# Performance work log

Measured on AMD Instinct MI355X. Metric: run time of the kernel, lower is better.

The kernel has to match this reference:

```python
import jax, jax.numpy as jnp
import numpy as np

K = 4          # deform conv kernel size
STRIDE = 4     # deform conv stride (no padding)
EPS = 1e-5     # BatchNorm eps
SLOPE = 0.01   # LeakyReLU default negative slope


def conv2d(x, w, b, stride):
    out = jax.lax.conv_general_dilated(
        x, w, (stride, stride), 'VALID',
        dimension_numbers=('NCHW', 'OIHW', 'NCHW'))
    return out + b[None, :, None, None]


def batchnorm(x, g, b, m, v):
    inv = g / jnp.sqrt(v + EPS)
    return x * inv[None, :, None, None] + (b - m * inv)[None, :, None, None]


def leaky_relu(x):
    return jnp.where(x >= 0, x, SLOPE * x)


def deform_conv(x, offset, w, b):
    # x: [B,C,H,W], offset: [B,2*K*K,Ho,Wo] with (dy,dx) interleaved per kernel tap
    B, C, H, W = x.shape
    Ho, Wo = offset.shape[2], offset.shape[3]
    KK = K * K
    off = offset.reshape(B, KK, 2, Ho, Wo)
    kh = jnp.repeat(jnp.arange(K), K).astype(x.dtype)   # [KK] kernel row
    kw = jnp.tile(jnp.arange(K), K).astype(x.dtype)     # [KK] kernel col
    base_y = (jnp.arange(Ho) * STRIDE).astype(x.dtype)
    base_x = (jnp.arange(Wo) * STRIDE).astype(x.dtype)
    # sampling coordinates [B,KK,Ho,Wo]
    py = base_y[None, None, :, None] + kh[None, :, None, None] + off[:, :, 0]
    px = base_x[None, None, None, :] + kw[None, :, None, None] + off[:, :, 1]
    y0 = jnp.floor(py)
    x0 = jnp.floor(px)
    wy = py - y0
    wx = px - x0

    def corner(yc, xc):
        yi = yc.astype(jnp.int32)
        xi = xc.astype(jnp.int32)
        valid = (yi >= 0) & (yi < H) & (xi >= 0) & (xi < W)
        yi = jnp.clip(yi, 0, H - 1)
        xi = jnp.clip(xi, 0, W - 1)
        # per-batch gather: [B,C,KK,Ho,Wo]
        v = jax.vmap(lambda img, a, c: img[:, a, c])(x, yi, xi)
        return v * valid[:, None].astype(x.dtype)

    v00 = corner(y0, x0)
    v01 = corner(y0, x0 + 1)
    v10 = corner(y0 + 1, x0)
    v11 = corner(y0 + 1, x0 + 1)
    wy_ = wy[:, None]
    wx_ = wx[:, None]
    sampled = (v00 * (1 - wy_) * (1 - wx_) + v01 * (1 - wy_) * wx_
               + v10 * wy_ * (1 - wx_) + v11 * wy_ * wx_)  # [B,C,KK,Ho,Wo]
    out = jnp.einsum('bckhw,ock->bohw', sampled, w.reshape(w.shape[0], C, KK))
    return out + b[None, :, None, None]


def setup_inputs() -> dict:
    key = jax.random.key(0)
    ks = jax.random.split(key, 16)
    f32 = jnp.float32
    inp = {
        'x': jax.random.normal(ks[0], (64, 3, 224, 224), f32),
        'stem_w': jax.random.normal(ks[1], (96, 3, 4, 4), f32) * 0.1,
        'stem_b': jax.random.normal(ks[2], (96,), f32) * 0.05,
        'bn1_g': jax.random.uniform(ks[3], (96,), f32, 0.5, 1.5),
        'bn1_b': jax.random.normal(ks[4], (96,), f32) * 0.05,
        'bn1_m': jax.random.normal(ks[5], (96,), f32) * 0.05,
        'bn1_v': jax.random.uniform(ks[6], (96,), f32, 0.5, 1.5),
        'off_w': jax.random.normal(ks[7], (32, 96, 4, 4), f32) * 0.02,
        'off_b': jax.random.normal(ks[8], (32,), f32) * 0.02,
        'dcn_w': jax.random.normal(ks[9], (768, 96, 4, 4), f32) * 0.05,
        'dcn_b': jax.random.normal(ks[10], (768,), f32) * 0.05,
        'bn2_g': jax.random.uniform(ks[11], (768,), f32, 0.5, 1.5),
        'bn2_b': jax.random.normal(ks[12], (768,), f32) * 0.05,
        'bn2_m': jax.random.normal(ks[13], (768,), f32) * 0.05,
        'bn2_v': jax.random.uniform(ks[14], (768,), f32, 0.5, 1.5),
    }
    return inp


def reference(x, stem_w, stem_b, bn1_g, bn1_b, bn1_m, bn1_v,
              off_w, off_b, dcn_w, dcn_b, bn2_g, bn2_b, bn2_m, bn2_v):
    h = conv2d(x, stem_w, stem_b, 4)                      # [B,96,56,56]
    h = leaky_relu(batchnorm(h, bn1_g, bn1_b, bn1_m, bn1_v))
    offset = conv2d(h, off_w, off_b, 4)                   # [B,32,14,14]
    h = deform_conv(h, offset, dcn_w, dcn_b)              # [B,768,14,14]
    h = leaky_relu(batchnorm(h, bn2_g, bn2_b, bn2_m, bn2_v))
    B, C, Ho, Wo = h.shape
    return h.reshape(B, C, Ho * Wo).transpose(0, 2, 1)    # [B,196,768]
```

## Files before the change

kernel.cpp:

```cpp
#include <hip/hip_runtime.h>

#define EPS   1e-5f
#define SLOPE 0.01f

#define WS_H1B  0L
#define WS_OFF  9633792L
#define WS_W1T  10035200L
#define WS_S1   10039808L
#define WS_T1   10039904L
#define WS_T2   10040000L
#define WS_SB   10040768L
#define WS_WTB  19674560L
#define WS_WOB  20264384L

__device__ __forceinline__ unsigned short f2bf(float f) {
    unsigned int u = __builtin_bit_cast(unsigned int, f);
    u += 0x7fffu + ((u >> 16) & 1u);
    return (unsigned short)(u >> 16);
}
__device__ __forceinline__ float bf2f(unsigned short u) {
    unsigned int t = ((unsigned int)u) << 16;
    return __builtin_bit_cast(float, t);
}

typedef __attribute__((ext_vector_type(4))) unsigned short ushort4v;
typedef __attribute__((ext_vector_type(8))) short bf16x8;
typedef __attribute__((ext_vector_type(4))) float floatx4;

__global__ __launch_bounds__(256) void k0_prep(
    const float* __restrict__ stem_w, const float* __restrict__ stem_b,
    const float* __restrict__ bn1_g,  const float* __restrict__ bn1_b,
    const float* __restrict__ bn1_m,  const float* __restrict__ bn1_v,
    const float* __restrict__ off_w,  const float* __restrict__ dcn_w,
    const float* __restrict__ dcn_b,  const float* __restrict__ bn2_g,
    const float* __restrict__ bn2_b,  const float* __restrict__ bn2_m,
    const float* __restrict__ bn2_v,  float* __restrict__ ws)
{
    long i = (long)blockIdx.x * 256 + threadIdx.x;
    unsigned short* Wtb = (unsigned short*)(ws + WS_WTB);
    unsigned short* Wob = (unsigned short*)(ws + WS_WOB);
    if (i < 1179648L) {
        int oc = (int)(i / 1536), k = (int)(i % 1536);
        int kk = k / 96, c = k % 96;
        float inv2 = bn2_g[oc] * rsqrtf(bn2_v[oc] + EPS);
        Wtb[i] = f2bf(dcn_w[oc * 1536 + c * 16 + kk] * inv2);
    } else if (i < 1228800L) {
        int i2 = (int)(i - 1179648L);
        int oc = i2 / 1536, k = i2 % 1536;
        int khw = k / 96, c = k % 96;
        Wob[i2] = f2bf(off_w[oc * 1536 + c * 16 + khw]);
    } else if (i < 1233408L) {
        int i3 = (int)(i - 1228800L);
        int k = i3 / 96, c = i3 % 96;
        ws[WS_W1T + i3] = stem_w[c * 48 + k];
    } else if (i < 1233504L) {
        int c = (int)(i - 1233408L);
        ws[WS_S1 + c] = bn1_g[c] * rsqrtf(bn1_v[c] + EPS);
    } else if (i < 1233600L) {
        int c = (int)(i - 1233504L);
        float s = bn1_g[c] * rsqrtf(bn1_v[c] + EPS);
        ws[WS_T1 + c] = stem_b[c] * s + bn1_b[c] - bn1_m[c] * s;
    } else if (i < 1234368L) {
        int oc = (int)(i - 1233600L);
        float inv2 = bn2_g[oc] * rsqrtf(bn2_v[oc] + EPS);
        ws[WS_T2 + oc] = dcn_b[oc] * inv2 + bn2_b[oc] - bn2_m[oc] * inv2;
    }
}

__global__ __launch_bounds__(384) void k1_stem(
    const float* __restrict__ x, const float* __restrict__ w1t,
    const float* __restrict__ s1, const float* __restrict__ t1,
    unsigned short* __restrict__ h1)
{
    const int oy = blockIdx.x;
    const int b  = blockIdx.y;
    const int tid = threadIdx.x;

    __shared__ float xs[3 * 4 * 224];
    __shared__ float wsh[48 * 100];
    __shared__ float s1s[96], t1s[96];

    for (int i = tid; i < 2688; i += 384) {
        int ci = i / 896, r = i % 896;
        int kh = r / 224, xx = r % 224;
        xs[i] = x[((long)(b * 3 + ci) * 224 + oy * 4 + kh) * 224 + xx];
    }
    for (int i = tid; i < 4608; i += 384) {
        int k = i / 96, c = i % 96;
        wsh[k * 100 + c] = w1t[i];
    }
    if (tid < 96) { s1s[tid] = s1[tid]; t1s[tid] = t1[tid]; }
    __syncthreads();

    if (tid < 336) {
        int oxg = tid / 24, cg = tid % 24;
        float acc[4][4] = {};
#pragma unroll
        for (int ci = 0; ci < 3; ci++) {
#pragma unroll
            for (int kh = 0; kh < 4; kh++) {
                const float* xrow = &xs[(ci * 4 + kh) * 224 + oxg * 16];
                float4 xv[4], wv[4];
#pragma unroll
                for (int o = 0; o < 4; o++) xv[o] = *(const float4*)&xrow[o * 4];
#pragma unroll
                for (int kw = 0; kw < 4; kw++)
                    wv[kw] = *(const float4*)&wsh[(ci * 16 + kh * 4 + kw) * 100 + cg * 4];
#pragma unroll
                for (int kw = 0; kw < 4; kw++) {
                    const float* wf = (const float*)&wv[kw];
#pragma unroll
                    for (int o = 0; o < 4; o++) {
                        float xv_s = ((const float*)&xv[o])[kw];
#pragma unroll
                        for (int cc = 0; cc < 4; cc++)
                            acc[o][cc] += xv_s * wf[cc];
                    }
                }
            }
        }
#pragma unroll
        for (int o = 0; o < 4; o++) {
            ushort4v hp;
#pragma unroll
            for (int cc = 0; cc < 4; cc++) {
                int c = cg * 4 + cc;
                float v = acc[o][cc] * s1s[c] + t1s[c];
                v = v >= 0.f ? v : SLOPE * v;
                ((unsigned short*)&hp)[cc] = f2bf(v);
            }
            *(ushort4v*)&h1[((long)((b * 56 + oy) * 56) + oxg * 4 + o) * 96 + cg * 4] = hp;
        }
    }
}

__global__ __launch_bounds__(256) void k2_mfma(
    const unsigned short* __restrict__ h1,
    const unsigned short* __restrict__ Wob,
    const float* __restrict__ off_b, float* __restrict__ off)
{
    const int tid  = threadIdx.x;
    const int wave = tid >> 6;
    const int lane = tid & 63;
    const int n0   = blockIdx.x * 128;
    const int m    = lane & 15;
    const int quad = lane >> 4;

    __shared__ unsigned short sA[128 * 32];
    __shared__ unsigned short sB[32 * 32];

    const int skoff = (lane & 3) * 8;
    int n_a = n0 + wave * 32 + (lane >> 2);
    int n_b = n_a + 16;
    int ba = n_a / 196, pa = n_a % 196;
    int bb = n_b / 196, pb = n_b % 196;
    long pixa = ((long)(ba * 56 + (pa / 14) * 4) * 56 + (pa % 14) * 4);
    long pixb = ((long)(bb * 56 + (pb / 14) * 4) * 56 + (pb % 14) * 4);

    const unsigned short* gB = Wob + (long)((wave & 1) * 16 + (lane >> 2)) * 1536 + skoff;
    unsigned short* lA0 = &sA[(wave * 32 +  0) * 32];
    unsigned short* lA1 = &sA[(wave * 32 + 16) * 32];
    unsigned short* lB  = &sB[((wave & 1) * 16) * 32];

    floatx4 acc[2][2];
#pragma unroll
    for (int i = 0; i < 2; i++)
#pragma unroll
        for (int j = 0; j < 2; j++) acc[i][j] = (floatx4)0.f;

    for (int kt = 0; kt < 48; ++kt) {
        int khw = kt / 3;
        int c0  = (kt - khw * 3) * 32;
        int kh  = khw >> 2, kw = khw & 3;
        long eoff = (long)(kh * 56 + kw) * 96 + c0 + skoff;
        const unsigned short* gA0 = h1 + pixa * 96 + eoff;
        const unsigned short* gA1 = h1 + pixb * 96 + eoff;

        __syncthreads();
        __builtin_amdgcn_global_load_lds(
            (const __attribute__((address_space(1))) void*)gA0,
            (__attribute__((address_space(3))) void*)lA0, 16, 0, 0);
        __builtin_amdgcn_global_load_lds(
            (const __attribute__((address_space(1))) void*)gA1,
            (__attribute__((address_space(3))) void*)lA1, 16, 0, 0);
        if (wave < 2)
            __builtin_amdgcn_global_load_lds(
                (const __attribute__((address_space(1))) void*)gB,
                (__attribute__((address_space(3))) void*)lB, 16, 0, 0);
        gB += 32;
        __syncthreads();

        bf16x8 af[2], bfr[2];
#pragma unroll
        for (int i = 0; i < 2; i++)
            af[i] = *(const bf16x8*)&sA[(wave * 32 + i * 16 + m) * 32 + quad * 8];
#pragma unroll
        for (int j = 0; j < 2; j++)
            bfr[j] = *(const bf16x8*)&sB[(j * 16 + m) * 32 + quad * 8];
#pragma unroll
        for (int i = 0; i < 2; i++)
#pragma unroll
            for (int j = 0; j < 2; j++)
                acc[i][j] = __builtin_amdgcn_mfma_f32_16x16x32_bf16(
                    af[i], bfr[j], acc[i][j], 0, 0, 0);
    }

    float tb[2];
#pragma unroll
    for (int j = 0; j < 2; j++) tb[j] = off_b[j * 16 + m];
#pragma unroll
    for (int i = 0; i < 2; i++)
#pragma unroll
        for (int r = 0; r < 4; r++) {
            long n = n0 + wave * 32 + i * 16 + quad * 4 + r;
#pragma unroll
            for (int j = 0; j < 2; j++)
                off[n * 32 + j * 16 + m] = acc[i][j][r] + tb[j];
        }
}

__global__ __launch_bounds__(384) void k3_sample(
    const unsigned short* __restrict__ h1, const float* __restrict__ off,
    unsigned short* __restrict__ S)
{
    const int p = blockIdx.x;
    const int b = blockIdx.y;
    const int y = p / 14, xo = p % 14;
    const int tid = threadIdx.x;
    const int c4 = tid % 24, kk = tid / 24;
    const int kh = kk >> 2, kw = kk & 3;

    const float* ob = off + ((long)(b * 196 + p)) * 32;
    float dy = ob[kk * 2];
    float dx = ob[kk * 2 + 1];

    float py = (float)(y * 4 + kh) + dy;
    float px = (float)(xo * 4 + kw) + dx;
    float y0f = floorf(py), x0f = floorf(px);
    float wy = py - y0f, wx = px - x0f;
    int y0 = (int)y0f, x0 = (int)x0f;
    int y1 = y0 + 1,  x1 = x0 + 1;

    float my0 = (y0 >= 0 && y0 < 56) ? 1.f : 0.f;
    float my1 = (y1 >= 0 && y1 < 56) ? 1.f : 0.f;
    float mx0 = (x0 >= 0 && x0 < 56) ? 1.f : 0.f;
    float mx1 = (x1 >= 0 && x1 < 56) ? 1.f : 0.f;
    int y0c = min(max(y0, 0), 55), y1c = min(max(y1, 0), 55);
    int x0c = min(max(x0, 0), 55), x1c = min(max(x1, 0), 55);

    const unsigned short* hb = h1 + (long)b * 56 * 56 * 96 + c4 * 4;
    ushort4v v00 = *(const ushort4v*)&hb[(y0c * 56 + x0c) * 96];
    ushort4v v01 = *(const ushort4v*)&hb[(y0c * 56 + x1c) * 96];
    ushort4v v10 = *(const ushort4v*)&hb[(y1c * 56 + x0c) * 96];
    ushort4v v11 = *(const ushort4v*)&hb[(y1c * 56 + x1c) * 96];

    float w00 = my0 * mx0 * (1.f - wy) * (1.f - wx);
    float w01 = my0 * mx1 * (1.f - wy) * wx;
    float w10 = my1 * mx0 * wy * (1.f - wx);
    float w11 = my1 * mx1 * wy * wx;

    ushort4v rr;
#pragma unroll
    for (int c = 0; c < 4; c++) {
        float v = bf2f(((unsigned short*)&v00)[c]) * w00
                + bf2f(((unsigned short*)&v01)[c]) * w01
                + bf2f(((unsigned short*)&v10)[c]) * w10
                + bf2f(((unsigned short*)&v11)[c]) * w11;
        ((unsigned short*)&rr)[c] = f2bf(v);
    }

    long n = (long)b * 196 + p;
    *(ushort4v*)&S[n * 1536 + kk * 96 + c4 * 4] = rr;
}

__global__ __launch_bounds__(256) void k4_gemm_mfma(
    const unsigned short* __restrict__ S,
    const unsigned short* __restrict__ Wtb,
    const float* __restrict__ t2, float* __restrict__ out)
{
    const int tid  = threadIdx.x;
    const int wave = tid >> 6;
    const int lane = tid & 63;
    const int oc0 = blockIdx.x * 128;
    const int n0  = blockIdx.y * 128;
    const int wr  = wave >> 1, wc = wave & 1;
    const int m    = lane & 15;
    const int quad = lane >> 4;

    __shared__ unsigned short sA[128 * 32];
    __shared__ unsigned short sB[128 * 32];

    const int srow  = wave * 32 + (lane >> 2);
    const int skoff = (lane & 3) * 8;
    const unsigned short* gA0 = S   + (long)(n0  + srow) * 1536 + skoff;
    const unsigned short* gA1 = gA0 + 16L * 1536;
    const unsigned short* gB0 = Wtb + (long)(oc0 + srow) * 1536 + skoff;
    const unsigned short* gB1 = gB0 + 16L * 1536;
    unsigned short* lA0 = &sA[(wave * 32 +  0) * 32];
    unsigned short* lA1 = &sA[(wave * 32 + 16) * 32];
    unsigned short* lB0 = &sB[(wave * 32 +  0) * 32];
    unsigned short* lB1 = &sB[(wave * 32 + 16) * 32];

    floatx4 acc[4][4];
#pragma unroll
    for (int i = 0; i < 4; i++)
#pragma unroll
        for (int j = 0; j < 4; j++) acc[i][j] = (floatx4)0.f;

    for (int kt = 0; kt < 48; ++kt) {
        __syncthreads();
        __builtin_amdgcn_global_load_lds(
            (const __attribute__((address_space(1))) void*)gA0,
            (__attribute__((address_space(3))) void*)lA0, 16, 0, 0);
        __builtin_amdgcn_global_load_lds(
            (const __attribute__((address_space(1))) void*)gA1,
            (__attribute__((address_space(3))) void*)lA1, 16, 0, 0);
        __builtin_amdgcn_global_load_lds(
            (const __attribute__((address_space(1))) void*)gB0,
            (__attribute__((address_space(3))) void*)lB0, 16, 0, 0);
        __builtin_amdgcn_global_load_lds(
            (const __attribute__((address_space(1))) void*)gB1,
            (__attribute__((address_space(3))) void*)lB1, 16, 0, 0);
        gA0 += 32; gA1 += 32; gB0 += 32; gB1 += 32;
        __syncthreads();

        bf16x8 af[4], bf[4];
#pragma unroll
        for (int i = 0; i < 4; i++)
            af[i] = *(const bf16x8*)&sA[(wr * 64 + i * 16 + m) * 32 + quad * 8];
#pragma unroll
        for (int j = 0; j < 4; j++)
            bf[j] = *(const bf16x8*)&sB[(wc * 64 + j * 16 + m) * 32 + quad * 8];
#pragma unroll
        for (int i = 0; i < 4; i++)
#pragma unroll
            for (int j = 0; j < 4; j++)
                acc[i][j] = __builtin_amdgcn_mfma_f32_16x16x32_bf16(
                    af[i], bf[j], acc[i][j], 0, 0, 0);
    }

    float tb[4];
#pragma unroll
    for (int j = 0; j < 4; j++) tb[j] = t2[oc0 + wc * 64 + j * 16 + m];
#pragma unroll
    for (int i = 0; i < 4; i++) {
#pragma unroll
        for (int r = 0; r < 4; r++) {
            long n = n0 + wr * 64 + i * 16 + quad * 4 + r;
            float* orow = out + n * 768 + oc0 + wc * 64 + m;
#pragma unroll
            for (int j = 0; j < 4; j++) {
                float v = acc[i][j][r] + tb[j];
                orow[j * 16] = v >= 0.f ? v : SLOPE * v;
            }
        }
    }
}

extern "C" void kernel_launch(void* const* d_in, const int* in_sizes, int n_in,
                              void* d_out, int out_size, void* d_ws, size_t ws_size,
                              hipStream_t stream)
{
    const float* x      = (const float*)d_in[0];
    const float* stem_w = (const float*)d_in[1];
    const float* stem_b = (const float*)d_in[2];
    const float* bn1_g  = (const float*)d_in[3];
    const float* bn1_b  = (const float*)d_in[4];
    const float* bn1_m  = (const float*)d_in[5];
    const float* bn1_v  = (const float*)d_in[6];
    const float* off_w  = (const float*)d_in[7];
    const float* off_b  = (const float*)d_in[8];
    const float* dcn_w  = (const float*)d_in[9];
    const float* dcn_b  = (const float*)d_in[10];
    const float* bn2_g  = (const float*)d_in[11];
    const float* bn2_b  = (const float*)d_in[12];
    const float* bn2_m  = (const float*)d_in[13];
    const float* bn2_v  = (const float*)d_in[14];

    float* ws  = (float*)d_ws;
    float* out = (float*)d_out;

    unsigned short* h1  = (unsigned short*)(ws + WS_H1B);
    float* off = ws + WS_OFF;
    float* w1t = ws + WS_W1T;
    float* s1  = ws + WS_S1;
    float* t1  = ws + WS_T1;
    float* t2  = ws + WS_T2;
    unsigned short* Sb  = (unsigned short*)(ws + WS_SB);
    unsigned short* Wtb = (unsigned short*)(ws + WS_WTB);
    unsigned short* Wob = (unsigned short*)(ws + WS_WOB);

    k0_prep<<<4823, 256, 0, stream>>>(stem_w, stem_b, bn1_g, bn1_b, bn1_m, bn1_v,
                                      off_w, dcn_w, dcn_b, bn2_g, bn2_b, bn2_m,
                                      bn2_v, ws);
    k1_stem<<<dim3(56, 64), 384, 0, stream>>>(x, w1t, s1, t1, h1);
    k2_mfma<<<98, 256, 0, stream>>>(h1, Wob, off_b, off);
    k3_sample<<<dim3(196, 64), 384, 0, stream>>>(h1, off, Sb);
    k4_gemm_mfma<<<dim3(6, 98), 256, 0, stream>>>(Sb, Wtb, t2, out);
}
```

Baseline: 252.7 us.

## Rewrite stem convolution as bf16 MFMA GEMM over 128-pixel tiles

Replaces the fp32 FMA-based stem conv with an implicit GEMM using 16x16x32 bf16 MFMA. Input patches are converted to bf16 into LDS, and weights are pre-packed in bf16 with K padded from 48 to 64 and loaded via global_load_lds. This moves the stem arithmetic from scalar FMAs onto matrix cores, at the cost of bf16 input rounding and scalar 2-byte stores of h1 that may be poorly coalesced.

```diff
diff --git a/kernel.cpp b/kernel.cpp
--- a/kernel.cpp
+++ b/kernel.cpp
@@ -5,13 +5,13 @@
 
 #define WS_H1B  0L
 #define WS_OFF  9633792L
-#define WS_W1T  10035200L
-#define WS_S1   10039808L
-#define WS_T1   10039904L
-#define WS_T2   10040000L
-#define WS_SB   10040768L
-#define WS_WTB  19674560L
-#define WS_WOB  20264384L
+#define WS_S1   10035200L
+#define WS_T1   10035296L
+#define WS_T2   10035392L
+#define WS_SB   10036160L
+#define WS_WTB  19669952L
+#define WS_WOB  20259776L
+#define WS_W1B  20284352L
 
 __device__ __forceinline__ unsigned short f2bf(float f) {
     unsigned int u = __builtin_bit_cast(unsigned int, f);
@@ -24,6 +24,7 @@
 }
 
 typedef __attribute__((ext_vector_type(4))) unsigned short ushort4v;
+typedef __attribute__((ext_vector_type(8))) unsigned short ushort8v;
 typedef __attribute__((ext_vector_type(8))) short bf16x8;
 typedef __attribute__((ext_vector_type(4))) float floatx4;
 
@@ -39,6 +40,7 @@
     long i = (long)blockIdx.x * 256 + threadIdx.x;
     unsigned short* Wtb = (unsigned short*)(ws + WS_WTB);
     unsigned short* Wob = (unsigned short*)(ws + WS_WOB);
+    unsigned short* W1b = (unsigned short*)(ws + WS_W1B);
     if (i < 1179648L) {
         int oc = (int)(i / 1536), k = (int)(i % 1536);
         int kk = k / 96, c = k % 96;
@@ -49,88 +51,109 @@
         int oc = i2 / 1536, k = i2 % 1536;
         int khw = k / 96, c = k % 96;
         Wob[i2] = f2bf(off_w[oc * 1536 + c * 16 + khw]);
-    } else if (i < 1233408L) {
+    } else if (i < 1234944L) {
         int i3 = (int)(i - 1228800L);
-        int k = i3 / 96, c = i3 % 96;
-        ws[WS_W1T + i3] = stem_w[c * 48 + k];
-    } else if (i < 1233504L) {
-        int c = (int)(i - 1233408L);
+        int ks = i3 / 3072, rr = i3 % 3072;
+        int oc = rr >> 5, kl = rr & 31;
+        int k  = ks * 32 + kl;
+        W1b[i3] = f2bf(k < 48 ? stem_w[oc * 48 + k] : 0.f);
+    } else if (i < 1235040L) {
+        int c = (int)(i - 1234944L);
         ws[WS_S1 + c] = bn1_g[c] * rsqrtf(bn1_v[c] + EPS);
-    } else if (i < 1233600L) {
-        int c = (int)(i - 1233504L);
+    } else if (i < 1235136L) {
+        int c = (int)(i - 1235040L);
         float s = bn1_g[c] * rsqrtf(bn1_v[c] + EPS);
         ws[WS_T1 + c] = stem_b[c] * s + bn1_b[c] - bn1_m[c] * s;
-    } else if (i < 1234368L) {
-        int oc = (int)(i - 1233600L);
+    } else if (i < 1235904L) {
+        int oc = (int)(i - 1235136L);
         float inv2 = bn2_g[oc] * rsqrtf(bn2_v[oc] + EPS);
         ws[WS_T2 + oc] = dcn_b[oc] * inv2 + bn2_b[oc] - bn2_m[oc] * inv2;
     }
 }
 
-__global__ __launch_bounds__(384) void k1_stem(
-    const float* __restrict__ x, const float* __restrict__ w1t,
+__global__ __launch_bounds__(256) void k1_stem_mfma(
+    const float* __restrict__ x, const unsigned short* __restrict__ W1b,
     const float* __restrict__ s1, const float* __restrict__ t1,
     unsigned short* __restrict__ h1)
 {
-    const int oy = blockIdx.x;
-    const int b  = blockIdx.y;
-    const int tid = threadIdx.x;
-
-    __shared__ float xs[3 * 4 * 224];
-    __shared__ float wsh[48 * 100];
-    __shared__ float s1s[96], t1s[96];
-
-    for (int i = tid; i < 2688; i += 384) {
-        int ci = i / 896, r = i % 896;
-        int kh = r / 224, xx = r % 224;
-        xs[i] = x[((long)(b * 3 + ci) * 224 + oy * 4 + kh) * 224 + xx];
-    }
-    for (int i = tid; i < 4608; i += 384) {
-        int k = i / 96, c = i % 96;
-        wsh[k * 100 + c] = w1t[i];
-    }
-    if (tid < 96) { s1s[tid] = s1[tid]; t1s[tid] = t1[tid]; }
+    const int tid  = threadIdx.x;
+    const int wave = tid >> 6, lane = tid & 63;
+    const int m = lane & 15, quad = lane >> 4;
+    const int p0 = blockIdx.x * 128;
+
+    __shared__ unsigned short sA[2][128][32];
+    __shared__ unsigned short sB[2][96][32];
+
+    {
+        unsigned short* sBf = &sB[0][0][0];
+#pragma unroll
+        for (int i = 0; i < 3; i++) {
+            int inst = wave * 3 + i;
+            const unsigned short* g = W1b + inst * 512 + lane * 8;
+            __builtin_amdgcn_global_load_lds(
+                (const __attribute__((address_space(1))) void*)g,
+                (__attribute__((address_space(3))) void*)(sBf + inst * 512),
+                16, 0, 0);
+        }
+    }
+
+    {
+        int r = tid >> 1, off = 16 + (tid & 1) * 8;
+        *(ushort8v*)&sA[1][r][off] = (ushort8v)0;
+    }
+
+#pragma unroll
+    for (int i = 0; i < 6; i++) {
+        int cid = tid + 256 * i;
+        int r = cid / 12, s = cid % 12;
+        int ci = s >> 2, kh = s & 3;
+        int p = p0 + r;
+        int b  = p / 3136, rem = p % 3136;
+        int oy = rem / 56, ox = rem % 56;
+        float4 v = *(const float4*)&x[((long)((b * 3 + ci) * 224 + oy * 4 + kh)) * 224 + ox * 4];
+        ushort4v hv;
+        hv.x = f2bf(v.x); hv.y = f2bf(v.y); hv.z = f2bf(v.z); hv.w = f2bf(v.w);
+        int k0i = ci * 16 + kh * 4;
+        *(ushort4v*)&sA[k0i >> 5][r][k0i & 31] = hv;
+    }
     __syncthreads();
 
-    if (tid < 336) {
-        int oxg = tid / 24, cg = tid % 24;
-        float acc[4][4] = {};
-#pragma unroll
-        for (int ci = 0; ci < 3; ci++) {
-#pragma unroll
-            for (int kh = 0; kh < 4; kh++) {
-                const float* xrow = &xs[(ci * 4 + kh) * 224 + oxg * 16];
-                float4 xv[4], wv[4];
-#pragma unroll
-                for (int o = 0; o < 4; o++) xv[o] = *(const float4*)&xrow[o * 4];
-#pragma unroll
-                for (int kw = 0; kw < 4; kw++)
-                    wv[kw] = *(const float4*)&wsh[(ci * 16 + kh * 4 + kw) * 100 + cg * 4];
-#pragma unroll
-                for (int kw = 0; kw < 4; kw++) {
-                    const float* wf = (const float*)&wv[kw];
-#pragma unroll
-                    for (int o = 0; o < 4; o++) {
-                        float xv_s = ((const float*)&xv[o])[kw];
-#pragma unroll
-                        for (int cc = 0; cc < 4; cc++)
-                            acc[o][cc] += xv_s * wf[cc];
-                    }
-                }
+    bf16x8 bfv[6][2], af[2][2];
+#pragma unroll
+    for (int j = 0; j < 6; j++)
+#pragma unroll
+        for (int ks = 0; ks < 2; ks++)
+            bfv[j][ks] = *(const bf16x8*)&sB[ks][j * 16 + m][quad * 8];
+#pragma unroll
+    for (int rt = 0; rt < 2; rt++)
+#pragma unroll
+        for (int ks = 0; ks < 2; ks++)
+            af[rt][ks] = *(const bf16x8*)&sA[ks][wave * 32 + rt * 16 + m][quad * 8];
+
+    floatx4 acc[2][6];
+#pragma unroll
+    for (int rt = 0; rt < 2; rt++)
+#pragma unroll
+        for (int j = 0; j < 6; j++) {
+            floatx4 a = (floatx4)0.f;
+            a = __builtin_amdgcn_mfma_f32_16x16x32_bf16(af[rt][0], bfv[j][0], a, 0, 0, 0);
+            a = __builtin_amdgcn_mfma_f32_16x16x32_bf16(af[rt][1], bfv[j][1], a, 0, 0, 0);
+            acc[rt][j] = a;
+        }
+
+#pragma unroll
+    for (int j = 0; j < 6; j++) {
+        int c = j * 16 + m;
+        float sc = s1[c], bi = t1[c];
+#pragma unroll
+        for (int rt = 0; rt < 2; rt++)
+#pragma unroll
+            for (int r = 0; r < 4; r++) {
+                long p = p0 + wave * 32 + rt * 16 + quad * 4 + r;
+                float v = acc[rt][j][r] * sc + bi;
+                v = v >= 0.f ? v : SLOPE * v;
+                h1[p * 96 + c] = f2bf(v);
             }
-        }
-#pragma unroll
-        for (int o = 0; o < 4; o++) {
-            ushort4v hp;
-#pragma unroll
-            for (int cc = 0; cc < 4; cc++) {
-                int c = cg * 4 + cc;
-                float v = acc[o][cc] * s1s[c] + t1s[c];
-                v = v >= 0.f ? v : SLOPE * v;
-                ((unsigned short*)&hp)[cc] = f2bf(v);
-            }
-            *(ushort4v*)&h1[((long)((b * 56 + oy) * 56) + oxg * 4 + o) * 96 + cg * 4] = hp;
-        }
     }
 }
 
@@ -382,18 +405,18 @@
 
     unsigned short* h1  = (unsigned short*)(ws + WS_H1B);
     float* off = ws + WS_OFF;
-    float* w1t = ws + WS_W1T;
     float* s1  = ws + WS_S1;
     float* t1  = ws + WS_T1;
     float* t2  = ws + WS_T2;
     unsigned short* Sb  = (unsigned short*)(ws + WS_SB);
     unsigned short* Wtb = (unsigned short*)(ws + WS_WTB);
     unsigned short* Wob = (unsigned short*)(ws + WS_WOB);
-
-    k0_prep<<<4823, 256, 0, stream>>>(stem_w, stem_b, bn1_g, bn1_b, bn1_m, bn1_v,
+    unsigned short* W1b = (unsigned short*)(ws + WS_W1B);
+
+    k0_prep<<<4828, 256, 0, stream>>>(stem_w, stem_b, bn1_g, bn1_b, bn1_m, bn1_v,
                                       off_w, dcn_w, dcn_b, bn2_g, bn2_b, bn2_m,
                                       bn2_v, ws);
-    k1_stem<<<dim3(56, 64), 384, 0, stream>>>(x, w1t, s1, t1, h1);
+    k1_stem_mfma<<<1568, 256, 0, stream>>>(x, W1b, s1, t1, h1);
     k2_mfma<<<98, 256, 0, stream>>>(h1, Wob, off_b, off);
     k3_sample<<<dim3(196, 64), 384, 0, stream>>>(h1, off, Sb);
     k4_gemm_mfma<<<dim3(6, 98), 256, 0, stream>>>(Sb, Wtb, t2, out);
```

Measured after the change: 223.3 us. 11.6% less time.
